# Optimization experiments

Hardware: AMD Instinct MI355X
Metric: run time of the kernel (lower is better)

Reference implementation:

```python
import jax, jax.numpy as jnp
import numpy as np

BH, S, D = 16, 2048, 128
TEMPERATURE = float(np.sqrt(D))


def setup_inputs() -> dict:
    key = jax.random.key(0)
    kq, kk, kv = jax.random.split(key, 3)
    q = jax.random.normal(kq, (BH, S, D), dtype=jnp.float32)
    k = jax.random.normal(kk, (BH, S, D), dtype=jnp.float32)
    v = jax.random.normal(kv, (BH, S, D), dtype=jnp.float32)
    # causal mask: True = masked (filled with -inf), broadcast to every batch*head
    causal = ~jnp.tril(jnp.ones((S, S), dtype=bool))
    mask = jnp.broadcast_to(causal, (BH, S, S))
    return {"q": q, "k": k, "v": v, "mask": mask}


def reference(q, k, v, mask):
    # attn = q @ k^T / temperature, masked_fill, softmax over keys, attn @ v
    attn = jnp.einsum("bqd,bkd->bqk", q, k) / TEMPERATURE  # [BH, S, S]
    attn = jnp.where(mask, -jnp.inf, attn)
    attn = jax.nn.softmax(attn, axis=2)
    # dropout is identity in eval mode
    output = jnp.einsum("bqk,bkd->bqd", attn, v)  # [BH, S, D]
    return (output, attn)
```

## Files before the change

### kernel.cpp

```cpp
#include <hip/hip_runtime.h>
#include <hip/hip_bf16.h>

#define BH_N 16
#define SEQ 2048
#define DH 128
#define PSTR 2056

typedef __attribute__((ext_vector_type(8))) short bf16x8;
typedef __attribute__((ext_vector_type(4))) float f32x4;

__device__ __forceinline__ short f2bf(float x) {
    union { __hip_bfloat16 b; short s; } u;
    u.b = __float2bfloat16(x);
    return u.s;
}
__device__ __forceinline__ float bf2f(unsigned short s) {
    union { unsigned int u; float f; } v;
    v.u = ((unsigned int)s) << 16;
    return v.f;
}

__global__ __launch_bounds__(256) void prep_kv(
    const float* __restrict__ kp, const float* __restrict__ vp,
    unsigned short* __restrict__ Kb, unsigned short* __restrict__ Vt)
{
    const int tid  = threadIdx.x;
    const int kb64 = blockIdx.x * 64;
    const int bh   = blockIdx.y;
    const float* Ksrc = kp + ((size_t)bh * SEQ + kb64) * DH;
    const float* Vsrc = vp + ((size_t)bh * SEQ + kb64) * DH;
    unsigned short* Kdst = Kb + ((size_t)bh * SEQ + kb64) * DH;
    unsigned short* Vdst = Vt + (size_t)bh * DH * SEQ + kb64;

    #pragma unroll
    for (int i = 0; i < 8; ++i) {
        const int f4 = i * 256 + tid;
        const float4 kv = *(const float4*)(Ksrc + (size_t)f4 * 4);
        ushort4 o;
        o.x = (unsigned short)f2bf(kv.x); o.y = (unsigned short)f2bf(kv.y);
        o.z = (unsigned short)f2bf(kv.z); o.w = (unsigned short)f2bf(kv.w);
        *(ushort4*)(Kdst + (size_t)f4 * 4) = o;
    }
    const int key   = tid & 63;
    const int dbase = (tid >> 6) * 4;
    #pragma unroll
    for (int j = 0; j < 8; ++j) {
        const int d0 = dbase + j * 16;
        const float4 vv = *(const float4*)(Vsrc + (size_t)key * DH + d0);
        Vdst[(size_t)(d0 + 0) * SEQ + key] = (unsigned short)f2bf(vv.x);
        Vdst[(size_t)(d0 + 1) * SEQ + key] = (unsigned short)f2bf(vv.y);
        Vdst[(size_t)(d0 + 2) * SEQ + key] = (unsigned short)f2bf(vv.z);
        Vdst[(size_t)(d0 + 3) * SEQ + key] = (unsigned short)f2bf(vv.w);
    }
}

#define LOADK4(K0, K1, K2, K3, KEYBASE) do {                                   \
    const unsigned short* kr_ = Kbh + (size_t)((KEYBASE) + c16) * DH + g * 8;  \
    K0 = *(const bf16x8*)(kr_);                                                \
    K1 = *(const bf16x8*)(kr_ + 32);                                           \
    K2 = *(const bf16x8*)(kr_ + 64);                                           \
    K3 = *(const bf16x8*)(kr_ + 96);                                           \
} while (0)

#define SW1(K0, K1, K2, K3, KEYBASE) do {                                      \
    f32x4 acc_ = {0.f, 0.f, 0.f, 0.f};                                         \
    acc_ = __builtin_amdgcn_mfma_f32_16x16x32_bf16(qf[0], K0, acc_, 0, 0, 0);  \
    acc_ = __builtin_amdgcn_mfma_f32_16x16x32_bf16(qf[1], K1, acc_, 0, 0, 0);  \
    acc_ = __builtin_amdgcn_mfma_f32_16x16x32_bf16(qf[2], K2, acc_, 0, 0, 0);  \
    acc_ = __builtin_amdgcn_mfma_f32_16x16x32_bf16(qf[3], K3, acc_, 0, 0, 0);  \
    const int key_ = (KEYBASE) + c16;                                          \
    const int qr_  = qw + g * 4;                                               \
    const float p0_ = (key_ <= qr_ + 0) ? __expf(acc_[0]) : 0.f;               \
    const float p1_ = (key_ <= qr_ + 1) ? __expf(acc_[1]) : 0.f;               \
    const float p2_ = (key_ <= qr_ + 2) ? __expf(acc_[2]) : 0.f;               \
    const float p3_ = (key_ <= qr_ + 3) ? __expf(acc_[3]) : 0.f;               \
    lsr[0] += p0_; lsr[1] += p1_; lsr[2] += p2_; lsr[3] += p3_;                \
    unsigned short* pq_ = &strip[g * 4][0] + key_;                             \
    pq_[0]        = (unsigned short)f2bf(p0_);                                 \
    pq_[PSTR]     = (unsigned short)f2bf(p1_);                                 \
    pq_[2 * PSTR] = (unsigned short)f2bf(p2_);                                 \
    pq_[3 * PSTR] = (unsigned short)f2bf(p3_);                                 \
} while (0)

#define LOADV8(V0,V1,V2,V3,V4,V5,V6,V7, KEYOFF) do {                           \
    const unsigned short* vb_ = Vbh + (size_t)c16 * SEQ + (KEYOFF) + g * 8;    \
    V0 = *(const bf16x8*)(vb_);                                                \
    V1 = *(const bf16x8*)(vb_ + 16 * SEQ);                                     \
    V2 = *(const bf16x8*)(vb_ + 32 * SEQ);                                     \
    V3 = *(const bf16x8*)(vb_ + 48 * SEQ);                                     \
    V4 = *(const bf16x8*)(vb_ + 64 * SEQ);                                     \
    V5 = *(const bf16x8*)(vb_ + 80 * SEQ);                                     \
    V6 = *(const bf16x8*)(vb_ + 96 * SEQ);                                     \
    V7 = *(const bf16x8*)(vb_ + 112 * SEQ);                                    \
} while (0)

#define PV8(PA, V0,V1,V2,V3,V4,V5,V6,V7) do {                                  \
    oacc[0] = __builtin_amdgcn_mfma_f32_16x16x32_bf16(PA, V0, oacc[0], 0, 0, 0); \
    oacc[1] = __builtin_amdgcn_mfma_f32_16x16x32_bf16(PA, V1, oacc[1], 0, 0, 0); \
    oacc[2] = __builtin_amdgcn_mfma_f32_16x16x32_bf16(PA, V2, oacc[2], 0, 0, 0); \
    oacc[3] = __builtin_amdgcn_mfma_f32_16x16x32_bf16(PA, V3, oacc[3], 0, 0, 0); \
    oacc[4] = __builtin_amdgcn_mfma_f32_16x16x32_bf16(PA, V4, oacc[4], 0, 0, 0); \
    oacc[5] = __builtin_amdgcn_mfma_f32_16x16x32_bf16(PA, V5, oacc[5], 0, 0, 0); \
    oacc[6] = __builtin_amdgcn_mfma_f32_16x16x32_bf16(PA, V6, oacc[6], 0, 0, 0); \
    oacc[7] = __builtin_amdgcn_mfma_f32_16x16x32_bf16(PA, V7, oacc[7], 0, 0, 0); \
} while (0)

__global__ __launch_bounds__(512, 4) void attn_main(
    const float* __restrict__ qp, const unsigned short* __restrict__ Kb,
    const unsigned short* __restrict__ Vt, float* __restrict__ outO,
    float* __restrict__ outA)
{
    __shared__ float lspart[8][16];
    __shared__ float lrec[16];
    __shared__ float Osh[16][132];
    __shared__ __align__(16) unsigned short strip[16][PSTR];

    const int b   = blockIdx.x;
    const int j   = b & 7;
    const int idx = b >> 3;
    const int bh  = 2 * j + (idx & 1);
    const int qt  = 127 - (idx >> 1);
    const int qw  = qt * 16;
    const size_t qbase = (size_t)bh * SEQ + qw;

    const int tid  = threadIdx.x;
    const int wv   = tid >> 6;
    const int lane = tid & 63;
    const int c16  = lane & 15;
    const int g    = lane >> 4;
    const float invT = 0.08838834764831845f;

    const unsigned short* Kbh = Kb + (size_t)bh * SEQ * DH;
    const unsigned short* Vbh = Vt + (size_t)bh * DH * SEQ;

    bf16x8 qf[4];
    {
        const float* qrow = qp + (qbase + c16) * DH + g * 8;
        #pragma unroll
        for (int c = 0; c < 4; ++c) {
            const float4 a = *(const float4*)(qrow + c * 32);
            const float4 bq = *(const float4*)(qrow + c * 32 + 4);
            bf16x8 f;
            f[0] = f2bf(a.x * invT);  f[1] = f2bf(a.y * invT);
            f[2] = f2bf(a.z * invT);  f[3] = f2bf(a.w * invT);
            f[4] = f2bf(bq.x * invT); f[5] = f2bf(bq.y * invT);
            f[6] = f2bf(bq.z * invT); f[7] = f2bf(bq.w * invT);
            qf[c] = f;
        }
    }

    float lsr[4] = {0.f, 0.f, 0.f, 0.f};
    const int n16 = qt + 1;
    {
        bf16x8 ka0, ka1, ka2, ka3, kb0, kb1, kb2, kb3;
        int t = wv;
        if (t < n16) LOADK4(ka0, ka1, ka2, ka3, t << 4);
        for (; t + 8 < n16; t += 16) {
            LOADK4(kb0, kb1, kb2, kb3, (t + 8) << 4);
            SW1(ka0, ka1, ka2, ka3, t << 4);
            if (t + 16 < n16) LOADK4(ka0, ka1, ka2, ka3, (t + 16) << 4);
            SW1(kb0, kb1, kb2, kb3, (t + 8) << 4);
        }
        if (t < n16) SW1(ka0, ka1, ka2, ka3, t << 4);
    }
    #pragma unroll
    for (int r = 0; r < 4; ++r) {
        float s = lsr[r];
        #pragma unroll
        for (int m = 1; m < 16; m <<= 1) s += __shfl_xor(s, m);
        lsr[r] = s;
    }
    if (c16 == 0) {
        #pragma unroll
        for (int r = 0; r < 4; ++r) lspart[wv][g * 4 + r] = lsr[r];
    }
    __syncthreads();
    float li[4];
    #pragma unroll
    for (int r = 0; r < 4; ++r) {
        float s = 0.f;
        #pragma unroll
        for (int w = 0; w < 8; ++w) s += lspart[w][g * 4 + r];
        li[r] = 1.f / s;
    }
    const int ns = (qw + 79) >> 6;
    if (wv == 0 && c16 == 0) {
        #pragma unroll
        for (int r = 0; r < 4; ++r) lrec[g * 4 + r] = li[r];
    }
    {
        const int row = tid >> 5;
        for (int c = n16 * 16 + (tid & 31); c < ns * 64; c += 32) strip[row][c] = 0;
    }
    __syncthreads();

    f32x4 oacc[8];
    #pragma unroll
    for (int d = 0; d < 8; ++d) oacc[d] = (f32x4){0.f, 0.f, 0.f, 0.f};

    {
        bf16x8 va0, va1, va2, va3, va4, va5, va6, va7;
        bf16x8 vb0, vb1, vb2, vb3, vb4, vb5, vb6, vb7;
        for (int S = wv; S < ns; S += 8) {
            const int KB = S << 6;
            LOADV8(va0,va1,va2,va3,va4,va5,va6,va7, KB);
            LOADV8(vb0,vb1,vb2,vb3,vb4,vb5,vb6,vb7, KB + 32);
            {
                const bf16x8 pa = *(const bf16x8*)(&strip[c16][KB + g * 8]);
                PV8(pa, va0,va1,va2,va3,va4,va5,va6,va7);
            }
            {
                const bf16x8 pa = *(const bf16x8*)(&strip[c16][KB + 32 + g * 8]);
                PV8(pa, vb0,vb1,vb2,vb3,vb4,vb5,vb6,vb7);
            }
        }
    }

    {
        const int valid = ns * 64;
        #pragma unroll
        for (int rr = 0; rr < 2; ++rr) {
            const int row = wv * 2 + rr;
            const float lr = lrec[row];
            float* orow = outA + (qbase + row) * SEQ;
            const unsigned short* srow = &strip[row][0];
            for (int c = lane * 4; c < SEQ; c += 256) {
                f32x4 w;
                if (c < valid) {
                    w[0] = bf2f(srow[c + 0]) * lr;
                    w[1] = bf2f(srow[c + 1]) * lr;
                    w[2] = bf2f(srow[c + 2]) * lr;
                    w[3] = bf2f(srow[c + 3]) * lr;
                } else {
                    w[0] = 0.f; w[1] = 0.f; w[2] = 0.f; w[3] = 0.f;
                }
                __builtin_nontemporal_store(w, (f32x4*)(orow + c));
            }
        }
    }

    for (int wp = 0; wp < 8; ++wp) {
        if (wv == wp) {
            #pragma unroll
            for (int dt = 0; dt < 8; ++dt) {
                #pragma unroll
                for (int r = 0; r < 4; ++r) {
                    const float val = oacc[dt][r] * li[r];
                    if (wp == 0) Osh[g * 4 + r][dt * 16 + c16]  = val;
                    else         Osh[g * 4 + r][dt * 16 + c16] += val;
                }
            }
        }
        __syncthreads();
    }
    {
        const int r  = tid >> 5;
        const int d0 = (tid & 31) * 4;
        float4 o;
        o.x = Osh[r][d0 + 0]; o.y = Osh[r][d0 + 1];
        o.z = Osh[r][d0 + 2]; o.w = Osh[r][d0 + 3];
        *(float4*)(outO + (qbase + r) * DH + d0) = o;
    }
}

__global__ __launch_bounds__(256) void attn_fallback(
    const float* __restrict__ qp, const float* __restrict__ kp,
    const float* __restrict__ vp, float* __restrict__ outO,
    float* __restrict__ outA)
{
    const int qt   = blockIdx.x;
    const int bh   = blockIdx.y;
    const int wv   = threadIdx.x >> 6;
    const int lane = threadIdx.x & 63;
    const int c16  = lane & 15;
    const int g    = lane >> 4;
    const int qw = qt * 64 + wv * 16;
    const size_t qbase = (size_t)bh * SEQ + qw;
    const float invT = 0.08838834764831845f;

    bf16x8 qf[4];
    {
        const float* qrow = qp + (qbase + c16) * DH + g * 8;
        #pragma unroll
        for (int c = 0; c < 4; ++c) {
            const float4 a = *(const float4*)(qrow + c * 32);
            const float4 bq = *(const float4*)(qrow + c * 32 + 4);
            bf16x8 f;
            f[0] = f2bf(a.x * invT);  f[1] = f2bf(a.y * invT);
            f[2] = f2bf(a.z * invT);  f[3] = f2bf(a.w * invT);
            f[4] = f2bf(bq.x * invT); f[5] = f2bf(bq.y * invT);
            f[6] = f2bf(bq.z * invT); f[7] = f2bf(bq.w * invT);
            qf[c] = f;
        }
    }
    const float* kbase = kp + (size_t)bh * SEQ * DH;
    const float* vbase = vp + (size_t)bh * SEQ * DH;

    float ls0 = 0.f, ls1 = 0.f, ls2 = 0.f, ls3 = 0.f;
    const int nkt16 = (qw + 16) >> 4;
    for (int t = 0; t < nkt16; ++t) {
        const int kb = t << 4;
        const float* krow = kbase + (size_t)(kb + c16) * DH + g * 8;
        f32x4 acc = {0.f, 0.f, 0.f, 0.f};
        #pragma unroll
        for (int c = 0; c < 4; ++c) {
            const float4 a = *(const float4*)(krow + c * 32);
            const float4 bq = *(const float4*)(krow + c * 32 + 4);
            bf16x8 f;
            f[0] = f2bf(a.x);  f[1] = f2bf(a.y);  f[2] = f2bf(a.z);  f[3] = f2bf(a.w);
            f[4] = f2bf(bq.x); f[5] = f2bf(bq.y); f[6] = f2bf(bq.z); f[7] = f2bf(bq.w);
            acc = __builtin_amdgcn_mfma_f32_16x16x32_bf16(qf[c], f, acc, 0, 0, 0);
        }
        const int key = kb + c16;
        const int qr  = qw + g * 4;
        if (key <= qr + 0) ls0 += __expf(acc[0]);
        if (key <= qr + 1) ls1 += __expf(acc[1]);
        if (key <= qr + 2) ls2 += __expf(acc[2]);
        if (key <= qr + 3) ls3 += __expf(acc[3]);
    }
    #pragma unroll
    for (int m = 1; m < 16; m <<= 1) {
        ls0 += __shfl_xor(ls0, m);
        ls1 += __shfl_xor(ls1, m);
        ls2 += __shfl_xor(ls2, m);
        ls3 += __shfl_xor(ls3, m);
    }
    const float li0 = 1.f / ls0, li1 = 1.f / ls1, li2 = 1.f / ls2, li3 = 1.f / ls3;

    __shared__ __align__(16) short ptileF[4][16][32];
    f32x4 oacc[8];
    #pragma unroll
    for (int d = 0; d < 8; ++d) oacc[d] = (f32x4){0.f, 0.f, 0.f, 0.f};

    const int n32 = (qw + 47) >> 5;
    for (int t = 0; t < n32; ++t) {
        const int kb32 = t << 5;
        #pragma unroll
        for (int h = 0; h < 2; ++h) {
            const int kb = kb32 + h * 16;
            const float* krow = kbase + (size_t)(kb + c16) * DH + g * 8;
            f32x4 acc = {0.f, 0.f, 0.f, 0.f};
            #pragma unroll
            for (int c = 0; c < 4; ++c) {
                const float4 a = *(const float4*)(krow + c * 32);
                const float4 bq = *(const float4*)(krow + c * 32 + 4);
                bf16x8 f;
                f[0] = f2bf(a.x);  f[1] = f2bf(a.y);  f[2] = f2bf(a.z);  f[3] = f2bf(a.w);
                f[4] = f2bf(bq.x); f[5] = f2bf(bq.y); f[6] = f2bf(bq.z); f[7] = f2bf(bq.w);
                acc = __builtin_amdgcn_mfma_f32_16x16x32_bf16(qf[c], f, acc, 0, 0, 0);
            }
            const int key = kb + c16;
            const int qr  = qw + g * 4;
            const float p0 = (key <= qr + 0) ? __expf(acc[0]) * li0 : 0.f;
            const float p1 = (key <= qr + 1) ? __expf(acc[1]) * li1 : 0.f;
            const float p2 = (key <= qr + 2) ? __expf(acc[2]) * li2 : 0.f;
            const float p3 = (key <= qr + 3) ? __expf(acc[3]) * li3 : 0.f;
            outA[(qbase + g * 4 + 0) * SEQ + kb + c16] = p0;
            outA[(qbase + g * 4 + 1) * SEQ + kb + c16] = p1;
            outA[(qbase + g * 4 + 2) * SEQ + kb + c16] = p2;
            outA[(qbase + g * 4 + 3) * SEQ + kb + c16] = p3;
            ptileF[wv][g * 4 + 0][h * 16 + c16] = f2bf(p0);
            ptileF[wv][g * 4 + 1][h * 16 + c16] = f2bf(p1);
            ptileF[wv][g * 4 + 2][h * 16 + c16] = f2bf(p2);
            ptileF[wv][g * 4 + 3][h * 16 + c16] = f2bf(p3);
        }
        bf16x8 pa = *(bf16x8*)&ptileF[wv][c16][g * 8];
        #pragma unroll
        for (int dt = 0; dt < 8; ++dt) {
            const float* vcol = vbase + (size_t)(kb32 + g * 8) * DH + dt * 16 + c16;
            bf16x8 vf;
            #pragma unroll
            for (int i = 0; i < 8; ++i) vf[i] = f2bf(vcol[(size_t)i * DH]);
            oacc[dt] = __builtin_amdgcn_mfma_f32_16x16x32_bf16(pa, vf, oacc[dt], 0, 0, 0);
        }
    }
    {
        const float4 z4 = {0.f, 0.f, 0.f, 0.f};
        float* zrow = outA + (qbase + (lane >> 2)) * SEQ;
        for (int c = n32 * 32 + (lane & 3) * 8; c < SEQ; c += 32) {
            *(float4*)(zrow + c)     = z4;
            *(float4*)(zrow + c + 4) = z4;
        }
    }
    #pragma unroll
    for (int dt = 0; dt < 8; ++dt) {
        #pragma unroll
        for (int r = 0; r < 4; ++r) {
            outO[(qbase + g * 4 + r) * DH + dt * 16 + c16] = oacc[dt][r];
        }
    }
}

extern "C" void kernel_launch(void* const* d_in, const int* in_sizes, int n_in,
                              void* d_out, int out_size, void* d_ws, size_t ws_size,
                              hipStream_t stream) {
    (void)in_sizes; (void)n_in; (void)out_size;
    const float* q = (const float*)d_in[0];
    const float* k = (const float*)d_in[1];
    const float* v = (const float*)d_in[2];
    float* outO = (float*)d_out;
    float* outA = outO + (size_t)BH_N * SEQ * DH;

    const size_t need = (size_t)BH_N * SEQ * DH * sizeof(unsigned short) * 2;
    if (ws_size >= need) {
        unsigned short* Kb = (unsigned short*)d_ws;
        unsigned short* Vt = Kb + (size_t)BH_N * SEQ * DH;
        prep_kv<<<dim3(SEQ / 64, BH_N), 256, 0, stream>>>(k, v, Kb, Vt);
        attn_main<<<dim3(2048), 512, 0, stream>>>(q, Kb, Vt, outO, outA);
    } else {
        attn_fallback<<<dim3(SEQ / 64, BH_N), 256, 0, stream>>>(q, k, v, outO, outA);
    }
}
```

Before: 164.1 us.

## Deepen K prefetch to four stages, software-pipeline V loads, split MFMA accumulators

Measured after the change: 168.9 us. +2.9%, slower.

```diff
diff --git a/kernel.cpp b/kernel.cpp
--- a/kernel.cpp
+++ b/kernel.cpp
@@ -63,17 +63,19 @@
 } while (0)
 
 #define SW1(K0, K1, K2, K3, KEYBASE) do {                                      \
-    f32x4 acc_ = {0.f, 0.f, 0.f, 0.f};                                         \
-    acc_ = __builtin_amdgcn_mfma_f32_16x16x32_bf16(qf[0], K0, acc_, 0, 0, 0);  \
-    acc_ = __builtin_amdgcn_mfma_f32_16x16x32_bf16(qf[1], K1, acc_, 0, 0, 0);  \
-    acc_ = __builtin_amdgcn_mfma_f32_16x16x32_bf16(qf[2], K2, acc_, 0, 0, 0);  \
-    acc_ = __builtin_amdgcn_mfma_f32_16x16x32_bf16(qf[3], K3, acc_, 0, 0, 0);  \
+    f32x4 accA_ = {0.f, 0.f, 0.f, 0.f};                                        \
+    f32x4 accB_ = {0.f, 0.f, 0.f, 0.f};                                        \
+    accA_ = __builtin_amdgcn_mfma_f32_16x16x32_bf16(qf[0], K0, accA_, 0, 0, 0);\
+    accB_ = __builtin_amdgcn_mfma_f32_16x16x32_bf16(qf[1], K1, accB_, 0, 0, 0);\
+    accA_ = __builtin_amdgcn_mfma_f32_16x16x32_bf16(qf[2], K2, accA_, 0, 0, 0);\
+    accB_ = __builtin_amdgcn_mfma_f32_16x16x32_bf16(qf[3], K3, accB_, 0, 0, 0);\
+    accA_ += accB_;                                                            \
     const int key_ = (KEYBASE) + c16;                                          \
     const int qr_  = qw + g * 4;                                               \
-    const float p0_ = (key_ <= qr_ + 0) ? __expf(acc_[0]) : 0.f;               \
-    const float p1_ = (key_ <= qr_ + 1) ? __expf(acc_[1]) : 0.f;               \
-    const float p2_ = (key_ <= qr_ + 2) ? __expf(acc_[2]) : 0.f;               \
-    const float p3_ = (key_ <= qr_ + 3) ? __expf(acc_[3]) : 0.f;               \
+    const float p0_ = (key_ <= qr_ + 0) ? __expf(accA_[0]) : 0.f;              \
+    const float p1_ = (key_ <= qr_ + 1) ? __expf(accA_[1]) : 0.f;              \
+    const float p2_ = (key_ <= qr_ + 2) ? __expf(accA_[2]) : 0.f;              \
+    const float p3_ = (key_ <= qr_ + 3) ? __expf(accA_[3]) : 0.f;              \
     lsr[0] += p0_; lsr[1] += p1_; lsr[2] += p2_; lsr[3] += p3_;                \
     unsigned short* pq_ = &strip[g * 4][0] + key_;                             \
     pq_[0]        = (unsigned short)f2bf(p0_);                                 \
@@ -152,16 +154,22 @@
     float lsr[4] = {0.f, 0.f, 0.f, 0.f};
     const int n16 = qt + 1;
     {
-        bf16x8 ka0, ka1, ka2, ka3, kb0, kb1, kb2, kb3;
+        bf16x8 kA0,kA1,kA2,kA3, kB0,kB1,kB2,kB3, kC0,kC1,kC2,kC3, kD0,kD1,kD2,kD3;
         int t = wv;
-        if (t < n16) LOADK4(ka0, ka1, ka2, ka3, t << 4);
-        for (; t + 8 < n16; t += 16) {
-            LOADK4(kb0, kb1, kb2, kb3, (t + 8) << 4);
-            SW1(ka0, ka1, ka2, ka3, t << 4);
-            if (t + 16 < n16) LOADK4(ka0, ka1, ka2, ka3, (t + 16) << 4);
-            SW1(kb0, kb1, kb2, kb3, (t + 8) << 4);
-        }
-        if (t < n16) SW1(ka0, ka1, ka2, ka3, t << 4);
+        if (t < n16)      LOADK4(kA0,kA1,kA2,kA3, t << 4);
+        if (t + 8 < n16)  LOADK4(kB0,kB1,kB2,kB3, (t + 8) << 4);
+        if (t + 16 < n16) LOADK4(kC0,kC1,kC2,kC3, (t + 16) << 4);
+        if (t + 24 < n16) LOADK4(kD0,kD1,kD2,kD3, (t + 24) << 4);
+        for (; t + 32 < n16; t += 32) {
+            SW1(kA0,kA1,kA2,kA3, t << 4);        LOADK4(kA0,kA1,kA2,kA3, (t + 32) << 4);
+            SW1(kB0,kB1,kB2,kB3, (t + 8) << 4);  LOADK4(kB0,kB1,kB2,kB3, (t + 40) << 4);
+            SW1(kC0,kC1,kC2,kC3, (t + 16) << 4); LOADK4(kC0,kC1,kC2,kC3, (t + 48) << 4);
+            SW1(kD0,kD1,kD2,kD3, (t + 24) << 4); LOADK4(kD0,kD1,kD2,kD3, (t + 56) << 4);
+        }
+        if (t < n16)      SW1(kA0,kA1,kA2,kA3, t << 4);
+        if (t + 8 < n16)  SW1(kB0,kB1,kB2,kB3, (t + 8) << 4);
+        if (t + 16 < n16) SW1(kC0,kC1,kC2,kC3, (t + 16) << 4);
+        if (t + 24 < n16) SW1(kD0,kD1,kD2,kD3, (t + 24) << 4);
     }
     #pragma unroll
     for (int r = 0; r < 4; ++r) {
@@ -201,18 +209,23 @@
     {
         bf16x8 va0, va1, va2, va3, va4, va5, va6, va7;
         bf16x8 vb0, vb1, vb2, vb3, vb4, vb5, vb6, vb7;
-        for (int S = wv; S < ns; S += 8) {
+        int S = wv;
+        if (S < ns) {
+            LOADV8(va0,va1,va2,va3,va4,va5,va6,va7, S << 6);
+            LOADV8(vb0,vb1,vb2,vb3,vb4,vb5,vb6,vb7, (S << 6) + 32);
+        }
+        for (; S < ns; S += 8) {
             const int KB = S << 6;
-            LOADV8(va0,va1,va2,va3,va4,va5,va6,va7, KB);
-            LOADV8(vb0,vb1,vb2,vb3,vb4,vb5,vb6,vb7, KB + 32);
             {
                 const bf16x8 pa = *(const bf16x8*)(&strip[c16][KB + g * 8]);
                 PV8(pa, va0,va1,va2,va3,va4,va5,va6,va7);
             }
+            if (S + 8 < ns) LOADV8(va0,va1,va2,va3,va4,va5,va6,va7, (S + 8) << 6);
             {
                 const bf16x8 pa = *(const bf16x8*)(&strip[c16][KB + 32 + g * 8]);
                 PV8(pa, vb0,vb1,vb2,vb3,vb4,vb5,vb6,vb7);
             }
+            if (S + 8 < ns) LOADV8(vb0,vb1,vb2,vb3,vb4,vb5,vb6,vb7, ((S + 8) << 6) + 32);
         }
     }
 
```
